# Kernel tuning notes

Measured on AMD Instinct MI355X. Metric: run time of the kernel, lower is better.

## Reference

```python
import jax, jax.numpy as jnp
import numpy as np

B = 4096   # batch
V = 512    # num_variables
H = 64     # hidden_dim


def setup_inputs() -> dict:
    key = jax.random.key(0)
    ks = jax.random.split(key, 6)
    return {
        "X": jax.random.normal(ks[0], (B, V), dtype=jnp.float32),
        "adjacency_logits": jax.random.normal(ks[1], (V, V), dtype=jnp.float32) * 0.1,
        # W1[i] is the first Linear of net i: maps V inputs -> H hidden
        "W1": jax.random.normal(ks[2], (V, V, H), dtype=jnp.float32) * (1.0 / np.sqrt(V)),
        "b1": jax.random.normal(ks[3], (V, H), dtype=jnp.float32) * 0.01,
        # W2[i] is the second Linear of net i: maps H hidden -> 1 output
        "W2": jax.random.normal(ks[4], (V, H), dtype=jnp.float32) * (1.0 / np.sqrt(H)),
        "b2": jax.random.normal(ks[5], (V,), dtype=jnp.float32) * 0.01,
    }


def reference(X, adjacency_logits, W1, b1, W2, b2):
    # Hard adjacency (hard_adjacency=True path): threshold sigmoid, zero diagonal.
    probs = jax.nn.sigmoid(adjacency_logits)
    adj = (probs > 0.5).astype(X.dtype) * (1.0 - jnp.eye(V, dtype=X.dtype))  # [V, V]

    # Original loop: for each i, net_i(X * adj[:, i]).
    # Fold the parent mask into the first-layer weights: W1_eff[i, v, h] = W1[i, v, h] * adj[v, i]
    W1_eff = W1 * adj.T[:, :, None]                      # [V, V, H]
    h = jax.nn.relu(jnp.einsum('bv,ivh->bih', X, W1_eff) + b1[None])  # [B, V, H]
    reconstructed = jnp.einsum('bih,ih->bi', h, W2) + b2[None]        # [B, V]
    return reconstructed, adj
```

## Files before the change

kernel.cpp:

```cpp
#include <hip/hip_runtime.h>
#include <hip/hip_bf16.h>
#include <stdint.h>

#define BB 4096
#define VV 512
#define HH 64

typedef short bf16x8 __attribute__((ext_vector_type(8)));
typedef float floatx4 __attribute__((ext_vector_type(4)));
typedef unsigned short ushort8 __attribute__((ext_vector_type(8)));

typedef const __attribute__((address_space(1))) void g_void;
typedef __attribute__((address_space(3))) void l_void;

__device__ __forceinline__ void gload_lds16(const void* g, void* l) {
    __builtin_amdgcn_global_load_lds((g_void*)g, (l_void*)l, 16, 0, 0);
}

__device__ __forceinline__ unsigned short f2bf_rne(float f) {
    unsigned int u = __float_as_uint(f);
    u += 0x7FFFu + ((u >> 16) & 1u);
    return (unsigned short)(u >> 16);
}

__global__ __launch_bounds__(256) void adj_kernel(const float* __restrict__ logits,
                                                  float* __restrict__ adj_out) {
    int idx = blockIdx.x * 256 + threadIdx.x;
    int v = idx >> 9, u = idx & (VV - 1);
    adj_out[idx] = (logits[idx] > 0.0f && v != u) ? 1.0f : 0.0f;
}

__global__ __launch_bounds__(256) void prep_fused_kernel(
        const float* __restrict__ X, const float* __restrict__ logits,
        const float* __restrict__ W1, float* __restrict__ adj_out,
        unsigned short* __restrict__ Xp, unsigned short* __restrict__ W1t) {
    __shared__ float tile[64][65];
    __shared__ float maskv[64];
    int bx = blockIdx.x;
    int t  = threadIdx.x;
    if (bx < 4096) {
        int i  = bx >> 3;
        int v0 = (bx & 7) << 6;
        if (t < 64) {
            int v = v0 + t;
            maskv[t] = (logits[(size_t)v * VV + i] > 0.0f && v != i) ? 1.0f : 0.0f;
        }
        const float4* src4 = (const float4*)(W1 + ((size_t)i * VV + v0) * HH);
        #pragma unroll
        for (int jj = 0; jj < 4; ++jj) {
            int c  = jj * 256 + t;
            int vr = c >> 4, h4 = c & 15;
            float4 w = src4[c];
            tile[vr][h4 * 4 + 0] = w.x;
            tile[vr][h4 * 4 + 1] = w.y;
            tile[vr][h4 * 4 + 2] = w.z;
            tile[vr][h4 * 4 + 3] = w.w;
        }
        __syncthreads();
        unsigned short* dst = W1t + (size_t)i * (HH * VV) + v0;
        #pragma unroll
        for (int j = 0; j < 2; ++j) {
            int c = j * 256 + t;
            int h = c >> 3;
            int vr0 = (c & 7) * 8;
            ushort8 o;
            #pragma unroll
            for (int r = 0; r < 8; ++r)
                o[r] = f2bf_rne(tile[vr0 + r][h] * maskv[vr0 + r]);
            *(ushort8*)&dst[(size_t)h * VV + vr0] = o;
        }
    } else {
        int idx = (bx - 4096) * 256 + t;
        {
            int v = idx >> 9, u = idx & (VV - 1);
            adj_out[idx] = (logits[idx] > 0.0f && v != u) ? 1.0f : 0.0f;
        }
        {
            int lane = idx & 63;
            int mt   = (idx >> 6) & 3;
            int ks   = (idx >> 8) & 15;
            int rb   = idx >> 12;
            int row  = rb * 64 + mt * 16 + (lane & 15);
            int k0   = ks * 32 + (lane >> 4) * 8;
            const float4* s4 = (const float4*)(X + (size_t)row * VV + k0);
            float4 a = s4[0], b = s4[1];
            ushort8 o;
            o[0] = f2bf_rne(a.x); o[1] = f2bf_rne(a.y);
            o[2] = f2bf_rne(a.z); o[3] = f2bf_rne(a.w);
            o[4] = f2bf_rne(b.x); o[5] = f2bf_rne(b.y);
            o[6] = f2bf_rne(b.z); o[7] = f2bf_rne(b.w);
            *(ushort8*)(Xp + (size_t)idx * 8) = o;
        }
    }
}

__global__ __launch_bounds__(256, 3) void dag_gemm_kernel(
        const unsigned short* __restrict__ Xp,
        const unsigned short* __restrict__ W1t,
        const float* __restrict__ b1,
        const float* __restrict__ W2,
        const float* __restrict__ b2,
        float* __restrict__ out)
{
    __shared__ __align__(16) unsigned short Ws[16384];
    __shared__ float Po[256];

    const int t    = threadIdx.x;
    const int wave = t >> 6;
    const int lane = t & 63;
    const int ln   = lane & 15;
    const int quad = lane >> 4;

    const int bx    = blockIdx.x;
    const int local = bx >> 3;
    const int i     = ((bx & 7) << 6) + (local >> 4);
    const int row0  = (local & 15) << 8;

    auto ldb = [&](int pos, int nt) -> bf16x8 {
        return *(const bf16x8*)&Ws[(nt * 16 + ln) * 256 + ((pos ^ (ln & 7)) * 8)];
    };

    const unsigned short* abase =
        Xp + (size_t)((row0 >> 6) + wave) * (64 * VV) + lane * 8;

    bf16x8 af[4][4];
    #pragma unroll
    for (int s = 0; s < 3; ++s)
        #pragma unroll
        for (int mt = 0; mt < 4; ++mt)
            af[s][mt] = *(const bf16x8*)(abase + (s * 4 + mt) * 512);

    const unsigned short* wbase = W1t + (size_t)i * (HH * VV);
    #pragma unroll
    for (int j = 0; j < 8; ++j) {
        int c = j * 256 + t;
        int h = c >> 5, s2 = c & 31;
        gload_lds16(wbase + (size_t)h * VV + (size_t)(s2 ^ (h & 7)) * 8,
                    (char*)Ws + c * 16);
    }
    __syncthreads();

    floatx4 acc[4][4];
    #pragma unroll
    for (int a = 0; a < 4; ++a)
        #pragma unroll
        for (int b = 0; b < 4; ++b)
            acc[a][b] = (floatx4){0.f, 0.f, 0.f, 0.f};

    bf16x8 bq[2][4];
    #pragma unroll
    for (int nt = 0; nt < 4; ++nt)
        bq[0][nt] = ldb(quad, nt);

    #pragma unroll
    for (int kk = 0; kk < 8; ++kk) {
        #pragma unroll
        for (int mt = 0; mt < 4; ++mt)
            af[(kk + 3) & 3][mt] =
                *(const bf16x8*)(abase + ((kk + 3) * 4 + mt) * 512);
        if (kk < 7) {
            #pragma unroll
            for (int nt = 0; nt < 4; ++nt)
                bq[(kk + 1) & 1][nt] = ldb((kk + 1) * 4 + quad, nt);
        }
        #pragma unroll
        for (int mt = 0; mt < 4; ++mt)
            #pragma unroll
            for (int nt = 0; nt < 4; ++nt)
                acc[mt][nt] = __builtin_amdgcn_mfma_f32_16x16x32_bf16(
                    af[kk & 3][mt], bq[kk & 1][nt], acc[mt][nt], 0, 0, 0);
    }

    __syncthreads();

    #pragma unroll
    for (int j = 0; j < 8; ++j) {
        int c = j * 256 + t;
        int h = c >> 5, s2 = c & 31;
        gload_lds16(wbase + (size_t)h * VV + (size_t)(32 + (s2 ^ (h & 7))) * 8,
                    (char*)Ws + c * 16);
    }
    __syncthreads();

    #pragma unroll
    for (int nt = 0; nt < 4; ++nt)
        bq[0][nt] = ldb(quad, nt);

    #pragma unroll
    for (int kk = 8; kk < 16; ++kk) {
        if (kk < 13) {
            #pragma unroll
            for (int mt = 0; mt < 4; ++mt)
                af[(kk + 3) & 3][mt] =
                    *(const bf16x8*)(abase + ((kk + 3) * 4 + mt) * 512);
        }
        if (kk < 15) {
            #pragma unroll
            for (int nt = 0; nt < 4; ++nt)
                bq[(kk + 1) & 1][nt] = ldb(((kk + 1) - 8) * 4 + quad, nt);
        }
        #pragma unroll
        for (int mt = 0; mt < 4; ++mt)
            #pragma unroll
            for (int nt = 0; nt < 4; ++nt)
                acc[mt][nt] = __builtin_amdgcn_mfma_f32_16x16x32_bf16(
                    af[kk & 3][mt], bq[kk & 1][nt], acc[mt][nt], 0, 0, 0);
    }

    float b1v[4], w2v[4];
    #pragma unroll
    for (int nt = 0; nt < 4; ++nt) {
        b1v[nt] = b1[i * HH + nt * 16 + ln];
        w2v[nt] = W2[i * HH + nt * 16 + ln];
    }
    const float b2i = b2[i];
    #pragma unroll
    for (int mt = 0; mt < 4; ++mt) {
        #pragma unroll
        for (int r = 0; r < 4; ++r) {
            float p = 0.f;
            #pragma unroll
            for (int nt = 0; nt < 4; ++nt) {
                float hv = acc[mt][nt][r] + b1v[nt];
                hv = hv > 0.f ? hv : 0.f;
                p += hv * w2v[nt];
            }
            p += __shfl_xor(p, 8);
            p += __shfl_xor(p, 4);
            p += __shfl_xor(p, 2);
            p += __shfl_xor(p, 1);
            if (ln == 0)
                Po[wave * 64 + mt * 16 + quad * 4 + r] = p + b2i;
        }
    }
    out[(size_t)(row0 + wave * 64 + lane) * VV + i] = Po[wave * 64 + lane];
}

__global__ __launch_bounds__(256) void fallback_kernel(
        const float* __restrict__ X, const float* __restrict__ logits,
        const float* __restrict__ W1, const float* __restrict__ b1,
        const float* __restrict__ W2, const float* __restrict__ b2,
        float* __restrict__ out) {
    __shared__ float Wc[128][64];
    int i   = blockIdx.x & (VV - 1);
    int row = (blockIdx.x >> 9) * 256 + threadIdx.x;
    float acc[64];
    #pragma unroll
    for (int h = 0; h < 64; ++h) acc[h] = 0.f;
    for (int v0 = 0; v0 < VV; v0 += 128) {
        __syncthreads();
        for (int j = 0; j < 32; ++j) {
            int idx = j * 256 + threadIdx.x;
            int vr = idx >> 6, h = idx & 63;
            int v = v0 + vr;
            float m = (logits[(size_t)v * VV + i] > 0.f && v != i) ? 1.f : 0.f;
            Wc[vr][h] = W1[((size_t)i * VV + v) * HH + h] * m;
        }
        __syncthreads();
        for (int vr = 0; vr < 128; ++vr) {
            float xv = X[(size_t)row * VV + v0 + vr];
            #pragma unroll
            for (int h = 0; h < 64; ++h) acc[h] += xv * Wc[vr][h];
        }
    }
    float p = b2[i];
    #pragma unroll
    for (int h = 0; h < 64; ++h) {
        float hv = acc[h] + b1[i * HH + h];
        p += (hv > 0.f ? hv : 0.f) * W2[i * HH + h];
    }
    out[(size_t)row * VV + i] = p;
}

extern "C" void kernel_launch(void* const* d_in, const int* in_sizes, int n_in,
                              void* d_out, int out_size, void* d_ws, size_t ws_size,
                              hipStream_t stream) {
    const float* X      = (const float*)d_in[0];
    const float* logits = (const float*)d_in[1];
    const float* W1     = (const float*)d_in[2];
    const float* b1     = (const float*)d_in[3];
    const float* W2     = (const float*)d_in[4];
    const float* b2     = (const float*)d_in[5];

    float* out     = (float*)d_out;
    float* adj_out = out + (size_t)BB * VV;

    const size_t xp_bytes  = (size_t)BB * VV * 2;
    const size_t w1t_bytes = (size_t)VV * HH * VV * 2;
    const size_t need = xp_bytes + w1t_bytes;

    if (ws_size >= need) {
        unsigned short* Xp  = (unsigned short*)d_ws;
        unsigned short* W1t = (unsigned short*)((char*)d_ws + xp_bytes);
        hipLaunchKernelGGL(prep_fused_kernel, dim3(5120), dim3(256), 0, stream,
                           X, logits, W1, adj_out, Xp, W1t);
        hipLaunchKernelGGL(dag_gemm_kernel, dim3(8192), dim3(256), 0, stream,
                           Xp, W1t, b1, W2, b2, out);
    } else {
        hipLaunchKernelGGL(adj_kernel, dim3((VV * VV) / 256), dim3(256), 0, stream,
                           logits, adj_out);
        hipLaunchKernelGGL(fallback_kernel, dim3(VV * (BB / 256)), dim3(256), 0, stream,
                           X, logits, W1, b1, W2, b2, out);
    }
}
```

Before: 256.7 us.

## Compute two output variables per block to reuse X fragments

Each block now handles two consecutive net indices i0 and i0+1, staging both W1 tiles in a doubled LDS buffer. Each X A-fragment loaded from global memory then feeds MFMAs for both nets, halving X traffic per output. The grid is halved and launch bounds drop to 2 blocks per CU. In exchange it doubles the accumulator registers and LDS per block, shortens X prefetch depth from 3 to 1 stage, and removes the blockIdx swizzle that improved L2 locality, which may reduce latency hiding.

```diff
diff --git a/kernel.cpp b/kernel.cpp
--- a/kernel.cpp
+++ b/kernel.cpp
@@ -94,7 +94,7 @@
     }
 }
 
-__global__ __launch_bounds__(256, 3) void dag_gemm_kernel(
+__global__ __launch_bounds__(256, 2) void dag_gemm_kernel(
         const unsigned short* __restrict__ Xp,
         const unsigned short* __restrict__ W1t,
         const float* __restrict__ b1,
@@ -102,8 +102,8 @@
         const float* __restrict__ b2,
         float* __restrict__ out)
 {
-    __shared__ __align__(16) unsigned short Ws[16384];
-    __shared__ float Po[256];
+    __shared__ __align__(16) unsigned short Ws[2][16384];
+    __shared__ float Po[2][256];
 
     const int t    = threadIdx.x;
     const int wave = t >> 6;
@@ -111,129 +111,145 @@
     const int ln   = lane & 15;
     const int quad = lane >> 4;
 
-    const int bx    = blockIdx.x;
-    const int local = bx >> 3;
-    const int i     = ((bx & 7) << 6) + (local >> 4);
-    const int row0  = (local & 15) << 8;
-
-    auto ldb = [&](int pos, int nt) -> bf16x8 {
-        return *(const bf16x8*)&Ws[(nt * 16 + ln) * 256 + ((pos ^ (ln & 7)) * 8)];
+    const int bx   = blockIdx.x;
+    const int i0   = (bx >> 4) << 1;
+    const int row0 = (bx & 15) << 8;
+
+    auto ldb = [&](int ii, int pos, int nt) -> bf16x8 {
+        return *(const bf16x8*)&Ws[ii][(nt * 16 + ln) * 256 + ((pos ^ (ln & 7)) * 8)];
     };
 
     const unsigned short* abase =
         Xp + (size_t)((row0 >> 6) + wave) * (64 * VV) + lane * 8;
 
-    bf16x8 af[4][4];
-    #pragma unroll
-    for (int s = 0; s < 3; ++s)
+    bf16x8 af[2][4];
+    #pragma unroll
+    for (int mt = 0; mt < 4; ++mt)
+        af[0][mt] = *(const bf16x8*)(abase + mt * 512);
+
+    const unsigned short* wb0 = W1t + (size_t)i0 * (HH * VV);
+    const unsigned short* wb1 = W1t + (size_t)(i0 + 1) * (HH * VV);
+    auto stage = [&](int kb) {
+        #pragma unroll
+        for (int j = 0; j < 8; ++j) {
+            int c = j * 256 + t;
+            int h = c >> 5, s2 = c & 31;
+            size_t off = (size_t)h * VV + (size_t)(kb + (s2 ^ (h & 7))) * 8;
+            gload_lds16(wb0 + off, (char*)&Ws[0][0] + c * 16);
+            gload_lds16(wb1 + off, (char*)&Ws[1][0] + c * 16);
+        }
+    };
+    stage(0);
+    __syncthreads();
+
+    floatx4 acc[2][4][4];
+    #pragma unroll
+    for (int ii = 0; ii < 2; ++ii)
+        #pragma unroll
+        for (int a = 0; a < 4; ++a)
+            #pragma unroll
+            for (int b = 0; b < 4; ++b)
+                acc[ii][a][b] = (floatx4){0.f, 0.f, 0.f, 0.f};
+
+    bf16x8 bq[2][2][4];
+    #pragma unroll
+    for (int ii = 0; ii < 2; ++ii)
+        #pragma unroll
+        for (int nt = 0; nt < 4; ++nt)
+            bq[0][ii][nt] = ldb(ii, quad, nt);
+
+    #pragma unroll
+    for (int kk = 0; kk < 8; ++kk) {
         #pragma unroll
         for (int mt = 0; mt < 4; ++mt)
-            af[s][mt] = *(const bf16x8*)(abase + (s * 4 + mt) * 512);
-
-    const unsigned short* wbase = W1t + (size_t)i * (HH * VV);
-    #pragma unroll
-    for (int j = 0; j < 8; ++j) {
-        int c = j * 256 + t;
-        int h = c >> 5, s2 = c & 31;
-        gload_lds16(wbase + (size_t)h * VV + (size_t)(s2 ^ (h & 7)) * 8,
-                    (char*)Ws + c * 16);
-    }
+            af[(kk + 1) & 1][mt] =
+                *(const bf16x8*)(abase + ((kk + 1) * 4 + mt) * 512);
+        if (kk < 7) {
+            #pragma unroll
+            for (int ii = 0; ii < 2; ++ii)
+                #pragma unroll
+                for (int nt = 0; nt < 4; ++nt)
+                    bq[(kk + 1) & 1][ii][nt] = ldb(ii, (kk + 1) * 4 + quad, nt);
+        }
+        #pragma unroll
+        for (int ii = 0; ii < 2; ++ii)
+            #pragma unroll
+            for (int mt = 0; mt < 4; ++mt)
+                #pragma unroll
+                for (int nt = 0; nt < 4; ++nt)
+                    acc[ii][mt][nt] = __builtin_amdgcn_mfma_f32_16x16x32_bf16(
+                        af[kk & 1][mt], bq[kk & 1][ii][nt], acc[ii][mt][nt], 0, 0, 0);
+    }
+
     __syncthreads();
 
-    floatx4 acc[4][4];
-    #pragma unroll
-    for (int a = 0; a < 4; ++a)
-        #pragma unroll
-        for (int b = 0; b < 4; ++b)
-            acc[a][b] = (floatx4){0.f, 0.f, 0.f, 0.f};
-
-    bf16x8 bq[2][4];
-    #pragma unroll
-    for (int nt = 0; nt < 4; ++nt)
-        bq[0][nt] = ldb(quad, nt);
-
-    #pragma unroll
-    for (int kk = 0; kk < 8; ++kk) {
-        #pragma unroll
-        for (int mt = 0; mt < 4; ++mt)
-            af[(kk + 3) & 3][mt] =
-                *(const bf16x8*)(abase + ((kk + 3) * 4 + mt) * 512);
-        if (kk < 7) {
-            #pragma unroll
-            for (int nt = 0; nt < 4; ++nt)
-                bq[(kk + 1) & 1][nt] = ldb((kk + 1) * 4 + quad, nt);
-        }
-        #pragma unroll
-        for (int mt = 0; mt < 4; ++mt)
-            #pragma unroll
-            for (int nt = 0; nt < 4; ++nt)
-                acc[mt][nt] = __builtin_amdgcn_mfma_f32_16x16x32_bf16(
-                    af[kk & 3][mt], bq[kk & 1][nt], acc[mt][nt], 0, 0, 0);
-    }
-
+    stage(32);
     __syncthreads();
 
     #pragma unroll
-    for (int j = 0; j < 8; ++j) {
-        int c = j * 256 + t;
-        int h = c >> 5, s2 = c & 31;
-        gload_lds16(wbase + (size_t)h * VV + (size_t)(32 + (s2 ^ (h & 7))) * 8,
-                    (char*)Ws + c * 16);
-    }
-    __syncthreads();
-
-    #pragma unroll
-    for (int nt = 0; nt < 4; ++nt)
-        bq[0][nt] = ldb(quad, nt);
+    for (int ii = 0; ii < 2; ++ii)
+        #pragma unroll
+        for (int nt = 0; nt < 4; ++nt)
+            bq[0][ii][nt] = ldb(ii, quad, nt);
 
     #pragma unroll
     for (int kk = 8; kk < 16; ++kk) {
-        if (kk < 13) {
+        if (kk < 15) {
             #pragma unroll
             for (int mt = 0; mt < 4; ++mt)
-                af[(kk + 3) & 3][mt] =
-                    *(const bf16x8*)(abase + ((kk + 3) * 4 + mt) * 512);
-        }
-        if (kk < 15) {
-            #pragma unroll
-            for (int nt = 0; nt < 4; ++nt)
-                bq[(kk + 1) & 1][nt] = ldb(((kk + 1) - 8) * 4 + quad, nt);
-        }
-        #pragma unroll
-        for (int mt = 0; mt < 4; ++mt)
-            #pragma unroll
-            for (int nt = 0; nt < 4; ++nt)
-                acc[mt][nt] = __builtin_amdgcn_mfma_f32_16x16x32_bf16(
-                    af[kk & 3][mt], bq[kk & 1][nt], acc[mt][nt], 0, 0, 0);
-    }
-
-    float b1v[4], w2v[4];
-    #pragma unroll
-    for (int nt = 0; nt < 4; ++nt) {
-        b1v[nt] = b1[i * HH + nt * 16 + ln];
-        w2v[nt] = W2[i * HH + nt * 16 + ln];
-    }
-    const float b2i = b2[i];
-    #pragma unroll
-    for (int mt = 0; mt < 4; ++mt) {
-        #pragma unroll
-        for (int r = 0; r < 4; ++r) {
-            float p = 0.f;
-            #pragma unroll
-            for (int nt = 0; nt < 4; ++nt) {
-                float hv = acc[mt][nt][r] + b1v[nt];
-                hv = hv > 0.f ? hv : 0.f;
-                p += hv * w2v[nt];
+                af[(kk + 1) & 1][mt] =
+                    *(const bf16x8*)(abase + ((kk + 1) * 4 + mt) * 512);
+            #pragma unroll
+            for (int ii = 0; ii < 2; ++ii)
+                #pragma unroll
+                for (int nt = 0; nt < 4; ++nt)
+                    bq[(kk + 1) & 1][ii][nt] = ldb(ii, ((kk + 1) - 8) * 4 + quad, nt);
+        }
+        #pragma unroll
+        for (int ii = 0; ii < 2; ++ii)
+            #pragma unroll
+            for (int mt = 0; mt < 4; ++mt)
+                #pragma unroll
+                for (int nt = 0; nt < 4; ++nt)
+                    acc[ii][mt][nt] = __builtin_amdgcn_mfma_f32_16x16x32_bf16(
+                        af[kk & 1][mt], bq[kk & 1][ii][nt], acc[ii][mt][nt], 0, 0, 0);
+    }
+
+    float b1v[2][4], w2v[2][4], b2i[2];
+    #pragma unroll
+    for (int ii = 0; ii < 2; ++ii) {
+        #pragma unroll
+        for (int nt = 0; nt < 4; ++nt) {
+            b1v[ii][nt] = b1[(i0 + ii) * HH + nt * 16 + ln];
+            w2v[ii][nt] = W2[(i0 + ii) * HH + nt * 16 + ln];
+        }
+        b2i[ii] = b2[i0 + ii];
+    }
+    #pragma unroll
+    for (int ii = 0; ii < 2; ++ii) {
+        #pragma unroll
+        for (int mt = 0; mt < 4; ++mt) {
+            #pragma unroll
+            for (int r = 0; r < 4; ++r) {
+                float p = 0.f;
+                #pragma unroll
+                for (int nt = 0; nt < 4; ++nt) {
+                    float hv = acc[ii][mt][nt][r] + b1v[ii][nt];
+                    hv = hv > 0.f ? hv : 0.f;
+                    p += hv * w2v[ii][nt];
+                }
+                p += __shfl_xor(p, 8);
+                p += __shfl_xor(p, 4);
+                p += __shfl_xor(p, 2);
+                p += __shfl_xor(p, 1);
+                if (ln == 0)
+                    Po[ii][wave * 64 + mt * 16 + quad * 4 + r] = p + b2i[ii];
             }
-            p += __shfl_xor(p, 8);
-            p += __shfl_xor(p, 4);
-            p += __shfl_xor(p, 2);
-            p += __shfl_xor(p, 1);
-            if (ln == 0)
-                Po[wave * 64 + mt * 16 + quad * 4 + r] = p + b2i;
-        }
-    }
-    out[(size_t)(row0 + wave * 64 + lane) * VV + i] = Po[wave * 64 + lane];
+        }
+    }
+    const int row = row0 + wave * 64 + lane;
+    out[(size_t)row * VV + i0]     = Po[0][wave * 64 + lane];
+    out[(size_t)row * VV + i0 + 1] = Po[1][wave * 64 + lane];
 }
 
 __global__ __launch_bounds__(256) void fallback_kernel(
@@ -294,7 +310,7 @@
         unsigned short* W1t = (unsigned short*)((char*)d_ws + xp_bytes);
         hipLaunchKernelGGL(prep_fused_kernel, dim3(5120), dim3(256), 0, stream,
                            X, logits, W1, adj_out, Xp, W1t);
-        hipLaunchKernelGGL(dag_gemm_kernel, dim3(8192), dim3(256), 0, stream,
+        hipLaunchKernelGGL(dag_gemm_kernel, dim3(4096), dim3(256), 0, stream,
                            Xp, W1t, b1, W2, b2, out);
     } else {
         hipLaunchKernelGGL(adj_kernel, dim3((VV * VV) / 256), dim3(256), 0, stream,
```

After: 244.6 us. -4.7%, faster.
